# Kernel optimization log

Hardware: AMD Instinct MI355X
Metric: run time of the kernel (lower is better)

## Reference

```python
import jax, jax.numpy as jnp
import numpy as np

EPS = 1e-8  # torch CosineSimilarity default eps

def setup_inputs() -> dict:
    key = jax.random.key(0)
    kv, kt, k1, k2, k3, k4 = jax.random.split(key, 6)
    B, S = 16, 1024
    VD, TD, H = 1024, 768, 512
    visual_features = jax.random.normal(kv, (B, S, VD), dtype=jnp.float32)
    text_features = jax.random.normal(kt, (B, S, TD), dtype=jnp.float32)
    # nn.Linear params: weight [out, in], bias [out]
    Wv = jax.random.normal(k1, (H, VD), dtype=jnp.float32) * (1.0 / np.sqrt(VD))
    bv = jax.random.normal(k2, (H,), dtype=jnp.float32) * 0.01
    Wt = jax.random.normal(k3, (H, TD), dtype=jnp.float32) * (1.0 / np.sqrt(TD))
    bt = jax.random.normal(k4, (H,), dtype=jnp.float32) * 0.01
    return {"visual_features": visual_features, "text_features": text_features,
            "Wv": Wv, "bv": bv, "Wt": Wt, "bt": bt}

def reference(visual_features, text_features, Wv, bv, Wt, bt):
    # Linear projections
    v = jnp.einsum('bsd,hd->bsh', visual_features, Wv) + bv  # [B,S,H]
    t = jnp.einsum('bsd,hd->bsh', text_features, Wt) + bt    # [B,S,H]
    # Cosine similarity matrix via normalized batched GEMM
    # (algebraically equal to broadcasting CosineSimilarity over (B,S,S,H))
    dots = jnp.einsum('bih,bjh->bij', v, t)                   # [B,S,S]
    vn = jnp.linalg.norm(v, axis=-1)                          # [B,S]
    tn = jnp.linalg.norm(t, axis=-1)                          # [B,S]
    denom = jnp.maximum(vn[:, :, None] * tn[:, None, :], EPS)
    return dots / denom
```

## Files before the change

kernel.cpp:

```cpp
#include <hip/hip_runtime.h>
#include <hip/hip_bf16.h>

typedef __bf16 bf16x8 __attribute__((ext_vector_type(8)));
typedef __bf16 bf16x4 __attribute__((ext_vector_type(4)));
typedef float  f32x4  __attribute__((ext_vector_type(4)));

#define MFMA16(a, b, c) __builtin_amdgcn_mfma_f32_16x16x32_bf16((a), (b), (c), 0, 0, 0)

#define BATCH 16
#define SEQ   1024
#define VD    1024
#define TD    768
#define HDIM  512
#define MROWS (BATCH * SEQ)

typedef __attribute__((address_space(1))) const unsigned int gas_uint;
typedef __attribute__((address_space(3))) unsigned int las_uint;

__device__ __forceinline__ void async_copy16(const void* g, void* l) {
    __builtin_amdgcn_global_load_lds((gas_uint*)g, (las_uint*)l, 16, 0, 0);
}

__device__ __forceinline__ void stage_tile256(const __bf16* __restrict__ src,
                                              size_t ld, int row0, int k0,
                                              __bf16* __restrict__ buf, int tid) {
#pragma unroll
    for (int i = 0; i < 4; ++i) {
        const int c = i * 512 + tid;
        const int r = c >> 3;
        const int g = (c & 7) ^ (r & 7);
        async_copy16(&src[(size_t)(row0 + r) * ld + k0 + g * 8],
                     &buf[(c & ~63) * 8]);
    }
}

__device__ __forceinline__ bf16x8 frag_read(const __bf16* __restrict__ buf,
                                            int r, int h, int fq) {
    return *reinterpret_cast<const bf16x8*>(&buf[(r * 8 + ((h * 4 + fq) ^ (r & 7))) * 8]);
}

__device__ __forceinline__ void ldA_f32(const float* __restrict__ src, int K,
                                        int row0, int k0, int tid, float4* regs) {
#pragma unroll
    for (int i = 0; i < 4; ++i) {
        const int c = i * 512 + tid;
        const int r = c >> 3;
        const int j = c & 7;
        const float4* p = reinterpret_cast<const float4*>(src) +
                          (size_t)(row0 + r) * (K >> 2) + (k0 >> 2) + j * 2;
        regs[i * 2]     = p[0];
        regs[i * 2 + 1] = p[1];
    }
}

__device__ __forceinline__ void stA_lds(__bf16* __restrict__ buf, int tid,
                                        const float4* regs) {
#pragma unroll
    for (int i = 0; i < 4; ++i) {
        const int c = i * 512 + tid;
        const int r = c >> 3;
        const int j = c & 7;
        const float4 x0 = regs[i * 2], x1 = regs[i * 2 + 1];
        bf16x8 q = {(__bf16)x0.x, (__bf16)x0.y, (__bf16)x0.z, (__bf16)x0.w,
                    (__bf16)x1.x, (__bf16)x1.y, (__bf16)x1.z, (__bf16)x1.w};
        *reinterpret_cast<bf16x8*>(&buf[(r * 8 + (j ^ (r & 7))) * 8]) = q;
    }
}

#define NC_WV (HDIM * VD / 4)
#define NC_WT (HDIM * TD / 4)
#define NW_PAIRS ((NC_WV + NC_WT) / 2)
#define CONVW_BLOCKS (NW_PAIRS / 256)
#define NZ_BLOCKS (2 * MROWS / 4 / 256)
#define CONVW_GRID (CONVW_BLOCKS + NZ_BLOCKS)

__global__ __launch_bounds__(256) void conv_w_kernel(
    const float* __restrict__ Wv, const float* __restrict__ Wt,
    __bf16* __restrict__ Wvb, __bf16* __restrict__ Wtb,
    float* __restrict__ n2z) {
    const int blk = blockIdx.x;
    if (blk >= CONVW_BLOCKS) {
        const int zi = (blk - CONVW_BLOCKS) * 256 + threadIdx.x;
        reinterpret_cast<float4*>(n2z)[zi] = float4{0.f, 0.f, 0.f, 0.f};
        return;
    }
    int k = (blk * 256 + threadIdx.x) * 2;
    const float* src;
    __bf16* dst;
    if (k < NC_WV) { src = Wv; dst = Wvb; }
    else { k -= NC_WV; src = Wt; dst = Wtb; }
    const float4 x0 = reinterpret_cast<const float4*>(src)[k];
    const float4 x1 = reinterpret_cast<const float4*>(src)[k + 1];
    bf16x8 q = {(__bf16)x0.x, (__bf16)x0.y, (__bf16)x0.z, (__bf16)x0.w,
                (__bf16)x1.x, (__bf16)x1.y, (__bf16)x1.z, (__bf16)x1.w};
    reinterpret_cast<bf16x8*>(dst)[k >> 1] = q;
}

__global__ __launch_bounds__(512, 2) void proj_kernel(
    const float* __restrict__ Xv32, const __bf16* __restrict__ Wvb, const float* __restrict__ bv_,
    const float* __restrict__ Xt32, const __bf16* __restrict__ Wtb, const float* __restrict__ bt_,
    __bf16* __restrict__ vout, __bf16* __restrict__ tout,
    float* __restrict__ vn2, float* __restrict__ tn2)
{
    __shared__ __bf16 As[2][256 * 64];
    __shared__ __bf16 Bs[2][256 * 64];

    const int L  = blockIdx.x;
    const int x  = L & 7;
    const int s  = L >> 3;
    const int z  = s >> 4;
    const int ss = s & 15;
    const int m0 = (x * 8 + (ss >> 1)) * 256;
    const int n0 = (ss & 1) * 256;

    const float* X; const __bf16* Wb; const float* bias; __bf16* out; float* n2; int K;
    if (z == 0) { X = Xv32; Wb = Wvb; bias = bv_; out = vout; n2 = vn2; K = VD; }
    else        { X = Xt32; Wb = Wtb; bias = bt_; out = tout; n2 = tn2; K = TD; }

    const int tid  = threadIdx.x;
    const int lane = tid & 63;
    const int wave = tid >> 6;
    const int wr   = wave >> 2;
    const int wc   = wave & 3;
    const int fr   = lane & 15;
    const int fq   = lane >> 4;

    f32x4 acc[8][4] = {};
    const int NKT = K >> 6;

    {
        float4 rA0[8], rA1[8];
        ldA_f32(X, K, m0, 0,  tid, rA0);
        ldA_f32(X, K, m0, 64, tid, rA1);
        stage_tile256(Wb, K, n0, 0,  Bs[0], tid);
        stage_tile256(Wb, K, n0, 64, Bs[1], tid);
        stA_lds(As[0], tid, rA0);
        stA_lds(As[1], tid, rA1);
        asm volatile("s_waitcnt vmcnt(4)" ::: "memory");
        asm volatile("s_waitcnt lgkmcnt(0)" ::: "memory");
        __builtin_amdgcn_s_barrier();
    }

    float4 regs[8];
    for (int kt = 0; kt < NKT; ++kt) {
        if (kt + 2 < NKT) {
            ldA_f32(X, K, m0, (kt + 2) << 6, tid, regs);
            __builtin_amdgcn_sched_barrier(0);
        }
        const __bf16* Ab = As[kt & 1];
        const __bf16* Bb = Bs[kt & 1];
        bf16x8 bfr[4][2];
#pragma unroll
        for (int q = 0; q < 4; ++q) {
            bf16x8 afr[2][2];
#pragma unroll
            for (int m2 = 0; m2 < 2; ++m2)
#pragma unroll
                for (int h = 0; h < 2; ++h)
                    afr[m2][h] = frag_read(Ab, wr * 128 + (q * 2 + m2) * 16 + fr, h, fq);
            if (q == 0) {
#pragma unroll
                for (int n = 0; n < 4; ++n)
#pragma unroll
                    for (int h = 0; h < 2; ++h)
                        bfr[n][h] = frag_read(Bb, wc * 64 + n * 16 + fr, h, fq);
            }
            __builtin_amdgcn_s_barrier();
            __builtin_amdgcn_s_setprio(1);
#pragma unroll
            for (int h = 0; h < 2; ++h)
#pragma unroll
                for (int m2 = 0; m2 < 2; ++m2)
#pragma unroll
                    for (int n = 0; n < 4; ++n)
                        acc[q * 2 + m2][n] = MFMA16(afr[m2][h], bfr[n][h], acc[q * 2 + m2][n]);
            __builtin_amdgcn_s_setprio(0);
        }
        if (kt < NKT - 1) {
            __builtin_amdgcn_s_barrier();
            __builtin_amdgcn_sched_barrier(0);
            if (kt + 2 < NKT) {
                stA_lds(As[kt & 1], tid, regs);
                stage_tile256(Wb, K, n0, (kt + 2) << 6, Bs[kt & 1], tid);
                asm volatile("s_waitcnt vmcnt(4)" ::: "memory");
            } else {
                asm volatile("s_waitcnt vmcnt(0)" ::: "memory");
            }
            asm volatile("s_waitcnt lgkmcnt(0)" ::: "memory");
            __builtin_amdgcn_sched_barrier(0);
            __builtin_amdgcn_s_barrier();
        }
    }

    float bc[4];
#pragma unroll
    for (int n = 0; n < 4; ++n)
        bc[n] = bias[n0 + wc * 64 + n * 16 + fr];

#pragma unroll
    for (int mf = 0; mf < 8; ++mf) {
        const int rowb = m0 + wr * 128 + mf * 16 + fq * 4;
#pragma unroll
        for (int r = 0; r < 4; ++r) {
            float s_ = 0.f;
#pragma unroll
            for (int n = 0; n < 4; ++n) {
                const float e = acc[mf][n][r] + bc[n];
                out[(size_t)(rowb + r) * HDIM + n0 + wc * 64 + n * 16 + fr] = (__bf16)e;
                s_ = fmaf(e, e, s_);
            }
            s_ += __shfl_xor(s_, 1);
            s_ += __shfl_xor(s_, 2);
            s_ += __shfl_xor(s_, 4);
            s_ += __shfl_xor(s_, 8);
            if (fr == 0) atomicAdd(&n2[rowb + r], s_);
        }
    }
}

__global__ __launch_bounds__(512, 2) void dots_kernel(const __bf16* __restrict__ v,
                                                      const __bf16* __restrict__ t,
                                                      const float* __restrict__ vn2,
                                                      const float* __restrict__ tn2,
                                                      float* __restrict__ out) {
    __shared__ __bf16 As[2][256 * 64];
    __shared__ __bf16 Bs[2][256 * 64];

    const int L  = blockIdx.x;
    const int x  = L & 7;
    const int s  = L >> 3;
    const int b  = x * 2 + (s >> 4);
    const int i0 = ((s >> 2) & 3) * 256;
    const int j0 = (s & 3) * 256;

    const __bf16* vb = v + (size_t)b * SEQ * HDIM;
    const __bf16* tb = t + (size_t)b * SEQ * HDIM;

    const int tid  = threadIdx.x;
    const int lane = tid & 63;
    const int wave = tid >> 6;
    const int wr   = wave >> 2;
    const int wc   = wave & 3;
    const int fr   = lane & 15;
    const int fq   = lane >> 4;

    f32x4 acc[8][4] = {};
    const int NKT = HDIM >> 6;

    stage_tile256(vb, HDIM, i0, 0,  As[0], tid);
    stage_tile256(tb, HDIM, j0, 0,  Bs[0], tid);
    stage_tile256(vb, HDIM, i0, 64, As[1], tid);
    stage_tile256(tb, HDIM, j0, 64, Bs[1], tid);
    asm volatile("s_waitcnt vmcnt(8)" ::: "memory");
    __builtin_amdgcn_s_barrier();

    for (int kt = 0; kt < NKT; ++kt) {
        const __bf16* Ab = As[kt & 1];
        const __bf16* Bb = Bs[kt & 1];
        bf16x8 bfr[4][2];
#pragma unroll
        for (int q = 0; q < 4; ++q) {
            bf16x8 afr[2][2];
#pragma unroll
            for (int m2 = 0; m2 < 2; ++m2)
#pragma unroll
                for (int h = 0; h < 2; ++h)
                    afr[m2][h] = frag_read(Ab, wr * 128 + (q * 2 + m2) * 16 + fr, h, fq);
            if (q == 0) {
#pragma unroll
                for (int n = 0; n < 4; ++n)
#pragma unroll
                    for (int h = 0; h < 2; ++h)
                        bfr[n][h] = frag_read(Bb, wc * 64 + n * 16 + fr, h, fq);
            }
            __builtin_amdgcn_s_barrier();
            __builtin_amdgcn_s_setprio(1);
#pragma unroll
            for (int h = 0; h < 2; ++h)
#pragma unroll
                for (int m2 = 0; m2 < 2; ++m2)
#pragma unroll
                    for (int n = 0; n < 4; ++n)
                        acc[q * 2 + m2][n] = MFMA16(afr[m2][h], bfr[n][h], acc[q * 2 + m2][n]);
            __builtin_amdgcn_s_setprio(0);
        }
        if (kt < NKT - 1) {
            __builtin_amdgcn_s_barrier();
            __builtin_amdgcn_sched_barrier(0);
            if (kt + 2 < NKT) {
                const int kk = (kt + 2) << 6;
                stage_tile256(vb, HDIM, i0, kk, As[kt & 1], tid);
                stage_tile256(tb, HDIM, j0, kk, Bs[kt & 1], tid);
                asm volatile("s_waitcnt vmcnt(8)" ::: "memory");
            } else {
                asm volatile("s_waitcnt vmcnt(0)" ::: "memory");
            }
            __builtin_amdgcn_sched_barrier(0);
            __builtin_amdgcn_s_barrier();
        }
    }

    float vr2[8][4];
#pragma unroll
    for (int mf = 0; mf < 8; ++mf)
#pragma unroll
        for (int r = 0; r < 4; ++r)
            vr2[mf][r] = vn2[b * SEQ + i0 + wr * 128 + mf * 16 + fq * 4 + r];

    float* outb = out + ((size_t)b << 20);
#pragma unroll
    for (int n = 0; n < 4; ++n) {
        const int j     = j0 + wc * 64 + n * 16 + fr;
        const float tj2 = tn2[b * SEQ + j];
#pragma unroll
        for (int mf = 0; mf < 8; ++mf) {
            const int ib = i0 + wr * 128 + mf * 16 + fq * 4;
#pragma unroll
            for (int r = 0; r < 4; ++r) {
                const float denom = fmaxf(sqrtf(vr2[mf][r] * tj2), 1e-8f);
                outb[(size_t)(ib + r) * SEQ + j] = acc[mf][n][r] * __builtin_amdgcn_rcpf(denom);
            }
        }
    }
}

extern "C" void kernel_launch(void* const* d_in, const int* in_sizes, int n_in,
                              void* d_out, int out_size, void* d_ws, size_t ws_size,
                              hipStream_t stream) {
    const float* Xv = (const float*)d_in[0];
    const float* Xt = (const float*)d_in[1];
    const float* Wv = (const float*)d_in[2];
    const float* bv = (const float*)d_in[3];
    const float* Wt = (const float*)d_in[4];
    const float* bt = (const float*)d_in[5];
    float* out = (float*)d_out;

    char* ws = (char*)d_ws;
    size_t off = 0;
    __bf16* v   = (__bf16*)(ws + off); off += (size_t)MROWS * HDIM * 2;
    __bf16* t   = (__bf16*)(ws + off); off += (size_t)MROWS * HDIM * 2;
    __bf16* Wvb = (__bf16*)(ws + off); off += (size_t)HDIM * VD * 2;
    __bf16* Wtb = (__bf16*)(ws + off); off += (size_t)HDIM * TD * 2;
    float*  vn2 = (float*)(ws + off);  off += (size_t)MROWS * 4;
    float*  tn2 = (float*)(ws + off);  off += (size_t)MROWS * 4;

    conv_w_kernel<<<CONVW_GRID, 256, 0, stream>>>(Wv, Wt, Wvb, Wtb, vn2);

    proj_kernel<<<256, 512, 0, stream>>>(Xv, Wvb, bv, Xt, Wtb, bt, v, t, vn2, tn2);

    dots_kernel<<<256, 512, 0, stream>>>(v, t, vn2, tn2, out);
}
```

Measured before the change: 236.9 us.

## Triple-buffer A tile and interleave fp32 load/convert with MFMA phases

Adds a third LDS buffer for the A (fp32 activation) tile. The global loads and bf16 conversion/LDS stores are split into four chunks, each issued inside one q-phase of the MFMA loop instead of in one bulk step before and after compute. The goal is to hide the fp32 load and convert latency behind matrix math and shorten the serialized tail between k-steps. It costs an extra 32KB of LDS, which may threaten the 2-blocks-per-CU occupancy, and it depends on careful vmcnt accounting.

Result: faster. 223.6 us (-5.6%).

```diff
diff --git a/kernel.cpp b/kernel.cpp
--- a/kernel.cpp
+++ b/kernel.cpp
@@ -39,32 +39,27 @@
     return *reinterpret_cast<const bf16x8*>(&buf[(r * 8 + ((h * 4 + fq) ^ (r & 7))) * 8]);
 }
 
-__device__ __forceinline__ void ldA_f32(const float* __restrict__ src, int K,
-                                        int row0, int k0, int tid, float4* regs) {
-#pragma unroll
-    for (int i = 0; i < 4; ++i) {
-        const int c = i * 512 + tid;
-        const int r = c >> 3;
-        const int j = c & 7;
-        const float4* p = reinterpret_cast<const float4*>(src) +
-                          (size_t)(row0 + r) * (K >> 2) + (k0 >> 2) + j * 2;
-        regs[i * 2]     = p[0];
-        regs[i * 2 + 1] = p[1];
-    }
-}
-
-__device__ __forceinline__ void stA_lds(__bf16* __restrict__ buf, int tid,
-                                        const float4* regs) {
-#pragma unroll
-    for (int i = 0; i < 4; ++i) {
-        const int c = i * 512 + tid;
-        const int r = c >> 3;
-        const int j = c & 7;
-        const float4 x0 = regs[i * 2], x1 = regs[i * 2 + 1];
-        bf16x8 q = {(__bf16)x0.x, (__bf16)x0.y, (__bf16)x0.z, (__bf16)x0.w,
-                    (__bf16)x1.x, (__bf16)x1.y, (__bf16)x1.z, (__bf16)x1.w};
-        *reinterpret_cast<bf16x8*>(&buf[(r * 8 + (j ^ (r & 7))) * 8]) = q;
-    }
+__device__ __forceinline__ void ldA_chunk(const float* __restrict__ src, int K,
+                                          int row0, int k0, int tid, int i,
+                                          float4* regs) {
+    const int c = i * 512 + tid;
+    const int r = c >> 3;
+    const int j = c & 7;
+    const float4* p = reinterpret_cast<const float4*>(src) +
+                      (size_t)(row0 + r) * (K >> 2) + (k0 >> 2) + j * 2;
+    regs[i * 2]     = p[0];
+    regs[i * 2 + 1] = p[1];
+}
+
+__device__ __forceinline__ void stA_chunk(__bf16* __restrict__ buf, int tid,
+                                          int i, const float4* regs) {
+    const int c = i * 512 + tid;
+    const int r = c >> 3;
+    const int j = c & 7;
+    const float4 x0 = regs[i * 2], x1 = regs[i * 2 + 1];
+    bf16x8 q = {(__bf16)x0.x, (__bf16)x0.y, (__bf16)x0.z, (__bf16)x0.w,
+                (__bf16)x1.x, (__bf16)x1.y, (__bf16)x1.z, (__bf16)x1.w};
+    *reinterpret_cast<bf16x8*>(&buf[(r * 8 + (j ^ (r & 7))) * 8]) = q;
 }
 
 #define NC_WV (HDIM * VD / 4)
@@ -102,7 +97,7 @@
     __bf16* __restrict__ vout, __bf16* __restrict__ tout,
     float* __restrict__ vn2, float* __restrict__ tn2)
 {
-    __shared__ __bf16 As[2][256 * 64];
+    __shared__ __bf16 As[3][256 * 64];
     __shared__ __bf16 Bs[2][256 * 64];
 
     const int L  = blockIdx.x;
@@ -128,27 +123,36 @@
     f32x4 acc[8][4] = {};
     const int NKT = K >> 6;
 
+    float4 regs[8];
     {
-        float4 rA0[8], rA1[8];
-        ldA_f32(X, K, m0, 0,  tid, rA0);
-        ldA_f32(X, K, m0, 64, tid, rA1);
+        float4 rA0[8];
+        ldA_chunk(X, K, m0, 0, tid, 0, rA0);
+        ldA_chunk(X, K, m0, 0, tid, 1, rA0);
+        ldA_chunk(X, K, m0, 0, tid, 2, rA0);
+        ldA_chunk(X, K, m0, 0, tid, 3, rA0);
         stage_tile256(Wb, K, n0, 0,  Bs[0], tid);
         stage_tile256(Wb, K, n0, 64, Bs[1], tid);
-        stA_lds(As[0], tid, rA0);
-        stA_lds(As[1], tid, rA1);
-        asm volatile("s_waitcnt vmcnt(4)" ::: "memory");
+        stA_chunk(As[0], tid, 0, rA0);
+        stA_chunk(As[0], tid, 1, rA0);
+        stA_chunk(As[0], tid, 2, rA0);
+        stA_chunk(As[0], tid, 3, rA0);
+        if (1 < NKT) {
+            ldA_chunk(X, K, m0, 64, tid, 0, regs);
+            ldA_chunk(X, K, m0, 64, tid, 1, regs);
+            ldA_chunk(X, K, m0, 64, tid, 2, regs);
+            ldA_chunk(X, K, m0, 64, tid, 3, regs);
+        }
+        asm volatile("s_waitcnt vmcnt(12)" ::: "memory");
         asm volatile("s_waitcnt lgkmcnt(0)" ::: "memory");
         __builtin_amdgcn_s_barrier();
     }
 
-    float4 regs[8];
+    int ar = 0, aw = 1;
     for (int kt = 0; kt < NKT; ++kt) {
-        if (kt + 2 < NKT) {
-            ldA_f32(X, K, m0, (kt + 2) << 6, tid, regs);
-            __builtin_amdgcn_sched_barrier(0);
-        }
-        const __bf16* Ab = As[kt & 1];
+        const __bf16* Ab = As[ar];
         const __bf16* Bb = Bs[kt & 1];
+        const int doW = (kt + 1 < NKT);
+        const int doL = (kt + 2 < NKT);
         bf16x8 bfr[4][2];
 #pragma unroll
         for (int q = 0; q < 4; ++q) {
@@ -165,6 +169,8 @@
                     for (int h = 0; h < 2; ++h)
                         bfr[n][h] = frag_read(Bb, wc * 64 + n * 16 + fr, h, fq);
             }
+            if (doW) stA_chunk(As[aw], tid, q, regs);
+            if (doL) ldA_chunk(X, K, m0, (kt + 2) << 6, tid, q, regs);
             __builtin_amdgcn_s_barrier();
             __builtin_amdgcn_s_setprio(1);
 #pragma unroll
@@ -180,15 +186,16 @@
             __builtin_amdgcn_s_barrier();
             __builtin_amdgcn_sched_barrier(0);
             if (kt + 2 < NKT) {
-                stA_lds(As[kt & 1], tid, regs);
                 stage_tile256(Wb, K, n0, (kt + 2) << 6, Bs[kt & 1], tid);
-                asm volatile("s_waitcnt vmcnt(4)" ::: "memory");
+                asm volatile("s_waitcnt vmcnt(12)" ::: "memory");
             } else {
                 asm volatile("s_waitcnt vmcnt(0)" ::: "memory");
             }
             asm volatile("s_waitcnt lgkmcnt(0)" ::: "memory");
             __builtin_amdgcn_sched_barrier(0);
             __builtin_amdgcn_s_barrier();
+            ar = aw;
+            aw = (aw == 2) ? 0 : aw + 1;
         }
     }
 
```
